# Performance work log

Hardware: AMD Instinct MI355X
Metric: run time of the kernel (lower is better)

## Reference

```python
import jax, jax.numpy as jnp
import numpy as np

N = 8192
IN_F = 256
OUT_F = 64
ALPHA = 0.3  # LeakyReLU negative slope
NEG_INF = -9e15


def setup_inputs() -> dict:
    key = jax.random.key(0)
    k1, k2, k3, k4 = jax.random.split(key, 4)
    h = jax.random.normal(k1, (N, IN_F), dtype=jnp.float32)
    # sparse-ish binary adjacency with self loops (values are 0/1 floats)
    adj = (jax.random.uniform(k2, (N, N)) < 0.05).astype(jnp.float32)
    adj = jnp.maximum(adj, jnp.eye(N, dtype=jnp.float32))
    # xavier_uniform-style scales (gain=1.414)
    w_lim = 1.414 * np.sqrt(6.0 / (IN_F + OUT_F))
    a_lim = 1.414 * np.sqrt(6.0 / (2 * OUT_F + 1))
    W = jax.random.uniform(k3, (IN_F, OUT_F), minval=-w_lim, maxval=w_lim, dtype=jnp.float32)
    a = jax.random.uniform(k4, (2 * OUT_F, 1), minval=-a_lim, maxval=a_lim, dtype=jnp.float32)
    return {"h": h, "adj": adj, "W": W, "a": a}


def reference(h, adj, W, a):
    # Wh: [N, F]
    Wh = h @ W
    # Additive decomposition of the original concat-attention:
    # e_ij = leakyrelu(a[:F].Wh_i + a[F:].Wh_j)  -- identical math, no NxNx2F tensor
    src = Wh @ a[:OUT_F]      # [N, 1]
    dst = Wh @ a[OUT_F:]      # [N, 1]
    e = jax.nn.leaky_relu(src + dst.T, negative_slope=ALPHA)  # [N, N]
    e = e * adj               # faithful: original multiplies by adj before masking
    att = jnp.where(adj > 0, e, NEG_INF)
    att = jax.nn.softmax(att, axis=1)
    # dropout omitted (eval mode / deterministic reference)
    h_prime = att @ Wh        # [N, F]
    return jax.nn.elu(h_prime)
```

## Files before the change

kernel.cpp:

```cpp
#include <hip/hip_runtime.h>
#include <hip/hip_bf16.h>

#define N_NODES 8192
#define IN_F    256
#define OUT_F   64
#define ALPHA   0.3f
#define MBIAS   20.0f
#define CSPL    8
#define COLS_PER (N_NODES / CSPL)
#define NTILES  (COLS_PER / 64)
#define LDP     72

typedef unsigned short u16;
typedef unsigned int   u32;
typedef __attribute__((ext_vector_type(8))) short bf16x8;
typedef __attribute__((ext_vector_type(4))) float f32x4;

__device__ __forceinline__ float bf2f(u32 u) { return __uint_as_float(u << 16); }
__device__ __forceinline__ u32 f2bfbits(float x) {
    u32 u = __float_as_uint(x);
    return (u + 0x7FFFu + ((u >> 16) & 1u)) >> 16;
}
__device__ __forceinline__ float lrelu(float s) { return s > 0.f ? s : ALPHA * s; }

template <bool BF16>
__device__ __forceinline__ float ld(const void* p, size_t idx) {
    if constexpr (BF16) return bf2f(((const u16*)p)[idx]);
    else                return ((const float*)p)[idx];
}

__global__ void gat_detect_kernel(const unsigned* __restrict__ adj_words,
                                  int* __restrict__ flag) {
    *flag = ((adj_words[0] & 0xFFFFu) == 0x3F80u) ? 1 : 0;
}

template <bool BF16>
__device__ __forceinline__ void wh4_impl(
    const void* __restrict__ h, const void* __restrict__ W,
    const void* __restrict__ a, float* __restrict__ src,
    float* __restrict__ dst, int i0, int lane, float* accv)
{
    float acc0 = 0.f, acc1 = 0.f, acc2 = 0.f, acc3 = 0.f;
#pragma unroll 8
    for (int k = 0; k < IN_F; ++k) {
        float wv = ld<BF16>(W, (size_t)k * OUT_F + lane);
        float h0 = ld<BF16>(h, (size_t)(i0 + 0) * IN_F + k);
        float h1 = ld<BF16>(h, (size_t)(i0 + 1) * IN_F + k);
        float h2 = ld<BF16>(h, (size_t)(i0 + 2) * IN_F + k);
        float h3 = ld<BF16>(h, (size_t)(i0 + 3) * IN_F + k);
        acc0 = fmaf(h0, wv, acc0);
        acc1 = fmaf(h1, wv, acc1);
        acc2 = fmaf(h2, wv, acc2);
        acc3 = fmaf(h3, wv, acc3);
    }
    float av = ld<BF16>(a, lane);
    float bv = ld<BF16>(a, OUT_F + lane);
    float accs[4] = {acc0, acc1, acc2, acc3};
#pragma unroll
    for (int r = 0; r < 4; ++r) {
        float ps = accs[r] * av, pd = accs[r] * bv;
#pragma unroll
        for (int off = 32; off > 0; off >>= 1) {
            ps += __shfl_xor(ps, off, 64);
            pd += __shfl_xor(pd, off, 64);
        }
        if (lane == 0) { src[i0 + r] = ps; dst[i0 + r] = pd; }
        accv[r] = accs[r];
    }
}

__global__ __launch_bounds__(256) void gat_wh_kernel(
    const void* __restrict__ h, const void* __restrict__ W,
    const void* __restrict__ a, const int* __restrict__ flag,
    u16* __restrict__ WhT, float* __restrict__ src, float* __restrict__ dst)
{
    __shared__ float accs[16][OUT_F];
    const int tid = threadIdx.x, wave = tid >> 6, lane = tid & 63;
    const int i0 = blockIdx.x * 16 + wave * 4;
    float av[4];
    if (*flag) wh4_impl<true >(h, W, a, src, dst, i0, lane, av);
    else       wh4_impl<false>(h, W, a, src, dst, i0, lane, av);
#pragma unroll
    for (int r = 0; r < 4; ++r) accs[wave * 4 + r][lane] = av[r];
    __syncthreads();
    if (tid < OUT_F) {
        u32 w[8];
#pragma unroll
        for (int e = 0; e < 8; ++e) {
            u32 lo = f2bfbits(accs[2 * e][tid]);
            u32 hi = f2bfbits(accs[2 * e + 1][tid]);
            w[e] = lo | (hi << 16);
        }
        u16* dstp = WhT + (size_t)tid * N_NODES + blockIdx.x * 16;
        *(uint4*)dstp       = *(uint4*)&w[0];
        *(uint4*)(dstp + 8) = *(uint4*)&w[4];
    }
}

template <bool BF16>
__device__ __forceinline__ u32 adj_mask16(const void* adjrow_base, int t)
{
    u32 msk = 0;
    if constexpr (BF16) {
        const uint4* p = (const uint4*)((const u16*)adjrow_base + t * 64);
        uint4 a0 = p[0], a1 = p[1];
        u32 aw[8] = {a0.x, a0.y, a0.z, a0.w, a1.x, a1.y, a1.z, a1.w};
#pragma unroll
        for (int e = 0; e < 8; ++e) {
            if (aw[e] & 0xFFFFu) msk |= (1u << (2 * e));
            if (aw[e] >> 16)     msk |= (1u << (2 * e + 1));
        }
    } else {
        const uint4* p = (const uint4*)((const float*)adjrow_base + t * 64);
        uint4 a0 = p[0], a1 = p[1], a2 = p[2], a3 = p[3];
        u32 aw[16] = {a0.x,a0.y,a0.z,a0.w, a1.x,a1.y,a1.z,a1.w,
                      a2.x,a2.y,a2.z,a2.w, a3.x,a3.y,a3.z,a3.w};
#pragma unroll
        for (int e = 0; e < 16; ++e)
            if (aw[e]) msk |= (1u << e);
    }
    return msk;
}

__global__ __launch_bounds__(256, 4) void gat_attn_kernel(
    const void* __restrict__ adj, const u16* __restrict__ WhT,
    const float* __restrict__ src, const float* __restrict__ dst,
    const int* __restrict__ flag,
    float* __restrict__ O_part, float* __restrict__ l_part)
{
    __shared__ alignas(16) u16 Plds[2][64 * LDP];
    __shared__ alignas(16) u16 Blds[2][64 * LDP];

    const int tid = threadIdx.x, wave = tid >> 6, lane = tid & 63;
    const int r = tid >> 2, cq = tid & 3;
    const int i0 = blockIdx.x * 64, c0 = blockIdx.y * COLS_PER;
    const int isbf = *flag;

    const float srow = src[i0 + r];
    const float m = lrelu(srow + MBIAS);

    const void* adjrow = isbf
        ? (const void*)((const u16*)adj + (size_t)(i0 + r) * N_NODES + c0 + cq * 16)
        : (const void*)((const float*)adj + (size_t)(i0 + r) * N_NODES + c0 + cq * 16);
    const u16*    whtrow = WhT + (size_t)r * N_NODES + c0 + cq * 16;
    const float4* dstp   = (const float4*)(dst + c0 + cq * 16);

    const int mrow = (lane & 15);
    const int kq   = (lane >> 4) * 8;
    const int pw   = r * LDP + cq * 16;

    f32x4 acc[4] = {{0,0,0,0},{0,0,0,0},{0,0,0,0},{0,0,0,0}};
    float lacc = 0.f;

    uint4  pb0, pb1;
    u32    pmsk;
    float4 pd0, pd1, pd2, pd3;

#define LOAD_TILE(t)                                                      \
    do {                                                                  \
        pb0 = *(const uint4*)(whtrow + (t) * 64);                         \
        pb1 = *(const uint4*)(whtrow + (t) * 64 + 8);                     \
        pmsk = isbf ? adj_mask16<true >(adjrow, (t))                      \
                    : adj_mask16<false>(adjrow, (t));                     \
        pd0 = dstp[(t) * 16];     pd1 = dstp[(t) * 16 + 1];               \
        pd2 = dstp[(t) * 16 + 2]; pd3 = dstp[(t) * 16 + 3];               \
    } while (0)

#define STAGE_TILE(buf)                                                   \
    do {                                                                  \
        *(uint4*)&Blds[buf][pw]     = pb0;                                \
        *(uint4*)&Blds[buf][pw + 8] = pb1;                                \
        float dv[16] = {pd0.x,pd0.y,pd0.z,pd0.w, pd1.x,pd1.y,pd1.z,pd1.w, \
                        pd2.x,pd2.y,pd2.z,pd2.w, pd3.x,pd3.y,pd3.z,pd3.w};\
        u32 po[8];                                                        \
        _Pragma("unroll")                                                 \
        for (int e = 0; e < 8; ++e) {                                     \
            float s0 = lrelu(srow + dv[2 * e]);                           \
            float s1 = lrelu(srow + dv[2 * e + 1]);                       \
            float p0 = (pmsk & (1u << (2 * e)))     ? __expf(s0 - m) : 0.f;\
            float p1 = (pmsk & (1u << (2 * e + 1))) ? __expf(s1 - m) : 0.f;\
            u32 q0 = f2bfbits(p0), q1 = f2bfbits(p1);                     \
            lacc += bf2f(q0) + bf2f(q1);            \
            po[e] = q0 | (q1 << 16);                                      \
        }                                                                 \
        *(uint4*)&Plds[buf][pw]     = *(uint4*)&po[0];                    \
        *(uint4*)&Plds[buf][pw + 8] = *(uint4*)&po[4];                    \
    } while (0)

    LOAD_TILE(0);
    STAGE_TILE(0);
    __syncthreads();

    for (int t = 0; t < NTILES; ++t) {
        const int cur = t & 1, nxt = cur ^ 1;
        if (t + 1 < NTILES) LOAD_TILE(t + 1);

#pragma unroll
        for (int ks = 0; ks < 2; ++ks) {
            bf16x8 avf = *(bf16x8*)&Plds[cur][(16 * wave + mrow) * LDP + ks * 32 + kq];
#pragma unroll
            for (int nt = 0; nt < 4; ++nt) {
                bf16x8 bvf = *(bf16x8*)&Blds[cur][(16 * nt + mrow) * LDP + ks * 32 + kq];
                acc[nt] = __builtin_amdgcn_mfma_f32_16x16x32_bf16(avf, bvf, acc[nt], 0, 0, 0);
            }
        }
        if (t + 1 < NTILES) STAGE_TILE(nxt);
        __syncthreads();
    }
#undef LOAD_TILE
#undef STAGE_TILE

    lacc += __shfl_xor(lacc, 1, 64);
    lacc += __shfl_xor(lacc, 2, 64);
    if (cq == 0) l_part[blockIdx.y * N_NODES + i0 + r] = lacc;

    float* Ob = O_part + (size_t)blockIdx.y * N_NODES * OUT_F;
#pragma unroll
    for (int nt = 0; nt < 4; ++nt)
#pragma unroll
        for (int reg = 0; reg < 4; ++reg) {
            int row = i0 + 16 * wave + (lane >> 4) * 4 + reg;
            int col = 16 * nt + (lane & 15);
            Ob[(size_t)row * OUT_F + col] = acc[nt][reg];
        }
}

__global__ __launch_bounds__(256) void gat_reduce_kernel(
    const float* __restrict__ O_part, const float* __restrict__ l_part,
    const int* __restrict__ flag, void* __restrict__ out)
{
    int gid = blockIdx.x * 256 + threadIdx.x;
    int i = gid >> 6;
    float O = 0.f, L = 0.f;
#pragma unroll
    for (int c = 0; c < CSPL; ++c) {
        O += O_part[(size_t)c * N_NODES * OUT_F + gid];
        L += l_part[c * N_NODES + i];
    }
    float hp = O / L;
    float o = hp > 0.f ? hp : expm1f(hp);
    if (*flag) ((u16*)out)[gid] = (u16)f2bfbits(o);
    else       ((float*)out)[gid] = o;
}

extern "C" void kernel_launch(void* const* d_in, const int* in_sizes, int n_in,
                              void* d_out, int out_size, void* d_ws, size_t ws_size,
                              hipStream_t stream)
{
    const void* h   = d_in[0];
    const void* adj = d_in[1];
    const void* W   = d_in[2];
    const void* a   = d_in[3];

    char* ws = (char*)d_ws;
    u16*   WhT    = (u16*)ws;
    float* src    = (float*)(ws + (1u << 20));
    float* dst    = (float*)(ws + (1u << 20) + 32768);
    int*   flag   = (int*)  (ws + (1u << 20) + 65536);
    float* O_part = (float*)(ws + (2u << 20));
    float* l_part = (float*)(ws + (18u << 20));

    gat_detect_kernel<<<1, 1, 0, stream>>>((const unsigned*)adj, flag);
    gat_wh_kernel<<<N_NODES / 16, 256, 0, stream>>>(h, W, a, flag, WhT, src, dst);
    dim3 grid(N_NODES / 64, CSPL);
    gat_attn_kernel<<<grid, 256, 0, stream>>>(adj, WhT, src, dst, flag, O_part, l_part);
    gat_reduce_kernel<<<N_NODES * OUT_F / 256, 256, 0, stream>>>(O_part, l_part, flag, d_out);
}
```

Measured before the change: 442.2 us.

## Shrink attention row tile to 32, drop double buffering, inline dtype detection

The attention kernel now processes 32 rows per block instead of 64. Each of the 8 threads per row handles 8 columns, and the four waves are split as 2 row-tiles by 2 column-pairs. The software-pipelined double-buffered LDS staging is replaced by a single buffer with two barriers per tile, and occupancy hints go from 4 to 8 blocks per CU. The separate detect kernel is removed and each kernel checks the adjacency dtype inline. The aim is more blocks and parallelism for the adj-bandwidth-bound loop and one fewer launch. The cost is that WhT tiles are reloaded by twice as many blocks and load latency is no longer overlapped with compute.

```diff
diff --git a/kernel.cpp b/kernel.cpp
--- a/kernel.cpp
+++ b/kernel.cpp
@@ -9,6 +9,7 @@
 #define CSPL    8
 #define COLS_PER (N_NODES / CSPL)
 #define NTILES  (COLS_PER / 64)
+#define ROWS    32
 #define LDP     72
 
 typedef unsigned short u16;
@@ -23,15 +24,14 @@
 }
 __device__ __forceinline__ float lrelu(float s) { return s > 0.f ? s : ALPHA * s; }
 
+__device__ __forceinline__ int detect_bf16(const void* adj) {
+    return ((((const u32*)adj)[0] & 0xFFFFu) == 0x3F80u) ? 1 : 0;
+}
+
 template <bool BF16>
 __device__ __forceinline__ float ld(const void* p, size_t idx) {
     if constexpr (BF16) return bf2f(((const u16*)p)[idx]);
     else                return ((const float*)p)[idx];
-}
-
-__global__ void gat_detect_kernel(const unsigned* __restrict__ adj_words,
-                                  int* __restrict__ flag) {
-    *flag = ((adj_words[0] & 0xFFFFu) == 0x3F80u) ? 1 : 0;
 }
 
 template <bool BF16>
@@ -71,15 +71,15 @@
 
 __global__ __launch_bounds__(256) void gat_wh_kernel(
     const void* __restrict__ h, const void* __restrict__ W,
-    const void* __restrict__ a, const int* __restrict__ flag,
+    const void* __restrict__ a, const void* __restrict__ adj,
     u16* __restrict__ WhT, float* __restrict__ src, float* __restrict__ dst)
 {
     __shared__ float accs[16][OUT_F];
     const int tid = threadIdx.x, wave = tid >> 6, lane = tid & 63;
     const int i0 = blockIdx.x * 16 + wave * 4;
     float av[4];
-    if (*flag) wh4_impl<true >(h, W, a, src, dst, i0, lane, av);
-    else       wh4_impl<false>(h, W, a, src, dst, i0, lane, av);
+    if (detect_bf16(adj)) wh4_impl<true >(h, W, a, src, dst, i0, lane, av);
+    else                  wh4_impl<false>(h, W, a, src, dst, i0, lane, av);
 #pragma unroll
     for (int r = 0; r < 4; ++r) accs[wave * 4 + r][lane] = av[r];
     __syncthreads();
@@ -97,137 +97,108 @@
     }
 }
 
-template <bool BF16>
-__device__ __forceinline__ u32 adj_mask16(const void* adjrow_base, int t)
-{
-    u32 msk = 0;
-    if constexpr (BF16) {
-        const uint4* p = (const uint4*)((const u16*)adjrow_base + t * 64);
-        uint4 a0 = p[0], a1 = p[1];
-        u32 aw[8] = {a0.x, a0.y, a0.z, a0.w, a1.x, a1.y, a1.z, a1.w};
-#pragma unroll
-        for (int e = 0; e < 8; ++e) {
-            if (aw[e] & 0xFFFFu) msk |= (1u << (2 * e));
-            if (aw[e] >> 16)     msk |= (1u << (2 * e + 1));
-        }
-    } else {
-        const uint4* p = (const uint4*)((const float*)adjrow_base + t * 64);
-        uint4 a0 = p[0], a1 = p[1], a2 = p[2], a3 = p[3];
-        u32 aw[16] = {a0.x,a0.y,a0.z,a0.w, a1.x,a1.y,a1.z,a1.w,
-                      a2.x,a2.y,a2.z,a2.w, a3.x,a3.y,a3.z,a3.w};
-#pragma unroll
-        for (int e = 0; e < 16; ++e)
-            if (aw[e]) msk |= (1u << e);
-    }
-    return msk;
-}
-
-__global__ __launch_bounds__(256, 4) void gat_attn_kernel(
+__global__ __launch_bounds__(256, 8) void gat_attn_kernel(
     const void* __restrict__ adj, const u16* __restrict__ WhT,
     const float* __restrict__ src, const float* __restrict__ dst,
-    const int* __restrict__ flag,
     float* __restrict__ O_part, float* __restrict__ l_part)
 {
-    __shared__ alignas(16) u16 Plds[2][64 * LDP];
-    __shared__ alignas(16) u16 Blds[2][64 * LDP];
+    __shared__ alignas(16) u16 Plds[ROWS * LDP];
+    __shared__ alignas(16) u16 Blds[64 * LDP];
 
     const int tid = threadIdx.x, wave = tid >> 6, lane = tid & 63;
-    const int r = tid >> 2, cq = tid & 3;
-    const int i0 = blockIdx.x * 64, c0 = blockIdx.y * COLS_PER;
-    const int isbf = *flag;
+    const int r  = tid >> 3, cq = tid & 7;
+    const int br = tid >> 2, bq = tid & 3;
+    const int i0 = blockIdx.x * ROWS, c0 = blockIdx.y * COLS_PER;
+    const int isbf = detect_bf16(adj);
 
     const float srow = src[i0 + r];
     const float m = lrelu(srow + MBIAS);
 
-    const void* adjrow = isbf
-        ? (const void*)((const u16*)adj + (size_t)(i0 + r) * N_NODES + c0 + cq * 16)
-        : (const void*)((const float*)adj + (size_t)(i0 + r) * N_NODES + c0 + cq * 16);
-    const u16*    whtrow = WhT + (size_t)r * N_NODES + c0 + cq * 16;
-    const float4* dstp   = (const float4*)(dst + c0 + cq * 16);
-
-    const int mrow = (lane & 15);
-    const int kq   = (lane >> 4) * 8;
-    const int pw   = r * LDP + cq * 16;
-
-    f32x4 acc[4] = {{0,0,0,0},{0,0,0,0},{0,0,0,0},{0,0,0,0}};
+    const u16*    whtrow = WhT + (size_t)br * N_NODES + c0 + bq * 16;
+    const float4* dstp   = (const float4*)(dst + c0 + cq * 8);
+    const u16*    adj16  = (const u16*)adj   + (size_t)(i0 + r) * N_NODES + c0 + cq * 8;
+    const float*  adj32  = (const float*)adj + (size_t)(i0 + r) * N_NODES + c0 + cq * 8;
+
+    const int mw = wave & 1, nw = wave >> 1;
+    const int mrow = lane & 15, kq = (lane >> 4) * 8;
+
+    f32x4 acc[2] = {{0,0,0,0},{0,0,0,0}};
     float lacc = 0.f;
 
-    uint4  pb0, pb1;
-    u32    pmsk;
-    float4 pd0, pd1, pd2, pd3;
-
-#define LOAD_TILE(t)                                                      \
-    do {                                                                  \
-        pb0 = *(const uint4*)(whtrow + (t) * 64);                         \
-        pb1 = *(const uint4*)(whtrow + (t) * 64 + 8);                     \
-        pmsk = isbf ? adj_mask16<true >(adjrow, (t))                      \
-                    : adj_mask16<false>(adjrow, (t));                     \
-        pd0 = dstp[(t) * 16];     pd1 = dstp[(t) * 16 + 1];               \
-        pd2 = dstp[(t) * 16 + 2]; pd3 = dstp[(t) * 16 + 3];               \
-    } while (0)
-
-#define STAGE_TILE(buf)                                                   \
-    do {                                                                  \
-        *(uint4*)&Blds[buf][pw]     = pb0;                                \
-        *(uint4*)&Blds[buf][pw + 8] = pb1;                                \
-        float dv[16] = {pd0.x,pd0.y,pd0.z,pd0.w, pd1.x,pd1.y,pd1.z,pd1.w, \
-                        pd2.x,pd2.y,pd2.z,pd2.w, pd3.x,pd3.y,pd3.z,pd3.w};\
-        u32 po[8];                                                        \
-        _Pragma("unroll")                                                 \
-        for (int e = 0; e < 8; ++e) {                                     \
-            float s0 = lrelu(srow + dv[2 * e]);                           \
-            float s1 = lrelu(srow + dv[2 * e + 1]);                       \
-            float p0 = (pmsk & (1u << (2 * e)))     ? __expf(s0 - m) : 0.f;\
-            float p1 = (pmsk & (1u << (2 * e + 1))) ? __expf(s1 - m) : 0.f;\
-            u32 q0 = f2bfbits(p0), q1 = f2bfbits(p1);                     \
-            lacc += bf2f(q0) + bf2f(q1);            \
-            po[e] = q0 | (q1 << 16);                                      \
-        }                                                                 \
-        *(uint4*)&Plds[buf][pw]     = *(uint4*)&po[0];                    \
-        *(uint4*)&Plds[buf][pw + 8] = *(uint4*)&po[4];                    \
-    } while (0)
-
-    LOAD_TILE(0);
-    STAGE_TILE(0);
-    __syncthreads();
-
     for (int t = 0; t < NTILES; ++t) {
-        const int cur = t & 1, nxt = cur ^ 1;
-        if (t + 1 < NTILES) LOAD_TILE(t + 1);
+        uint4 b0 = *(const uint4*)(whtrow + t * 64);
+        uint4 b1 = *(const uint4*)(whtrow + t * 64 + 8);
+        *(uint4*)&Blds[br * LDP + bq * 16]     = b0;
+        *(uint4*)&Blds[br * LDP + bq * 16 + 8] = b1;
+
+        u32 msk = 0;
+        if (isbf) {
+            uint4 av = *(const uint4*)(adj16 + t * 64);
+            u32 aw[4] = {av.x, av.y, av.z, av.w};
+#pragma unroll
+            for (int e = 0; e < 4; ++e) {
+                if (aw[e] & 0xFFFFu) msk |= (1u << (2 * e));
+                if (aw[e] >> 16)     msk |= (1u << (2 * e + 1));
+            }
+        } else {
+            uint4 a0 = *(const uint4*)(adj32 + t * 64);
+            uint4 a1 = *(const uint4*)(adj32 + t * 64 + 4);
+            u32 aw[8] = {a0.x,a0.y,a0.z,a0.w, a1.x,a1.y,a1.z,a1.w};
+#pragma unroll
+            for (int e = 0; e < 8; ++e)
+                if (aw[e]) msk |= (1u << e);
+        }
+        float4 d0 = dstp[t * 16], d1 = dstp[t * 16 + 1];
+        float dv[8] = {d0.x,d0.y,d0.z,d0.w, d1.x,d1.y,d1.z,d1.w};
+        u32 po[4];
+#pragma unroll
+        for (int e = 0; e < 4; ++e) {
+            float s0 = lrelu(srow + dv[2 * e]);
+            float s1 = lrelu(srow + dv[2 * e + 1]);
+            float p0 = (msk & (1u << (2 * e)))     ? __expf(s0 - m) : 0.f;
+            float p1 = (msk & (1u << (2 * e + 1))) ? __expf(s1 - m) : 0.f;
+            u32 q0 = f2bfbits(p0), q1 = f2bfbits(p1);
+            lacc += bf2f(q0) + bf2f(q1);
+            po[e] = q0 | (q1 << 16);
+        }
+        *(uint4*)&Plds[r * LDP + cq * 8] = *(uint4*)&po[0];
+
+        __syncthreads();
 
 #pragma unroll
         for (int ks = 0; ks < 2; ++ks) {
-            bf16x8 avf = *(bf16x8*)&Plds[cur][(16 * wave + mrow) * LDP + ks * 32 + kq];
-#pragma unroll
-            for (int nt = 0; nt < 4; ++nt) {
-                bf16x8 bvf = *(bf16x8*)&Blds[cur][(16 * nt + mrow) * LDP + ks * 32 + kq];
-                acc[nt] = __builtin_amdgcn_mfma_f32_16x16x32_bf16(avf, bvf, acc[nt], 0, 0, 0);
+            bf16x8 avf = *(bf16x8*)&Plds[(16 * mw + mrow) * LDP + ks * 32 + kq];
+#pragma unroll
+            for (int nt2 = 0; nt2 < 2; ++nt2) {
+                int nt = nw * 2 + nt2;
+                bf16x8 bvf = *(bf16x8*)&Blds[(16 * nt + mrow) * LDP + ks * 32 + kq];
+                acc[nt2] = __builtin_amdgcn_mfma_f32_16x16x32_bf16(avf, bvf, acc[nt2], 0, 0, 0);
             }
         }
-        if (t + 1 < NTILES) STAGE_TILE(nxt);
         __syncthreads();
     }
-#undef LOAD_TILE
-#undef STAGE_TILE
 
     lacc += __shfl_xor(lacc, 1, 64);
     lacc += __shfl_xor(lacc, 2, 64);
+    lacc += __shfl_xor(lacc, 4, 64);
     if (cq == 0) l_part[blockIdx.y * N_NODES + i0 + r] = lacc;
 
     float* Ob = O_part + (size_t)blockIdx.y * N_NODES * OUT_F;
 #pragma unroll
-    for (int nt = 0; nt < 4; ++nt)
+    for (int nt2 = 0; nt2 < 2; ++nt2) {
+        int nt = nw * 2 + nt2;
 #pragma unroll
         for (int reg = 0; reg < 4; ++reg) {
-            int row = i0 + 16 * wave + (lane >> 4) * 4 + reg;
+            int row = i0 + 16 * mw + (lane >> 4) * 4 + reg;
             int col = 16 * nt + (lane & 15);
-            Ob[(size_t)row * OUT_F + col] = acc[nt][reg];
-        }
+            Ob[(size_t)row * OUT_F + col] = acc[nt2][reg];
+        }
+    }
 }
 
 __global__ __launch_bounds__(256) void gat_reduce_kernel(
     const float* __restrict__ O_part, const float* __restrict__ l_part,
-    const int* __restrict__ flag, void* __restrict__ out)
+    const void* __restrict__ adj, void* __restrict__ out)
 {
     int gid = blockIdx.x * 256 + threadIdx.x;
     int i = gid >> 6;
@@ -239,8 +210,8 @@
     }
     float hp = O / L;
     float o = hp > 0.f ? hp : expm1f(hp);
-    if (*flag) ((u16*)out)[gid] = (u16)f2bfbits(o);
-    else       ((float*)out)[gid] = o;
+    if (detect_bf16(adj)) ((u16*)out)[gid] = (u16)f2bfbits(o);
+    else                  ((float*)out)[gid] = o;
 }
 
 extern "C" void kernel_launch(void* const* d_in, const int* in_sizes, int n_in,
@@ -256,13 +227,11 @@
     u16*   WhT    = (u16*)ws;
     float* src    = (float*)(ws + (1u << 20));
     float* dst    = (float*)(ws + (1u << 20) + 32768);
-    int*   flag   = (int*)  (ws + (1u << 20) + 65536);
     float* O_part = (float*)(ws + (2u << 20));
     float* l_part = (float*)(ws + (18u << 20));
 
-    gat_detect_kernel<<<1, 1, 0, stream>>>((const unsigned*)adj, flag);
-    gat_wh_kernel<<<N_NODES / 16, 256, 0, stream>>>(h, W, a, flag, WhT, src, dst);
-    dim3 grid(N_NODES / 64, CSPL);
-    gat_attn_kernel<<<grid, 256, 0, stream>>>(adj, WhT, src, dst, flag, O_part, l_part);
-    gat_reduce_kernel<<<N_NODES * OUT_F / 256, 256, 0, stream>>>(O_part, l_part, flag, d_out);
-}
+    gat_wh_kernel<<<N_NODES / 16, 256, 0, stream>>>(h, W, a, adj, WhT, src, dst);
+    dim3 grid(N_NODES / ROWS, CSPL);
+    gat_attn_kernel<<<grid, 256, 0, stream>>>(adj, WhT, src, dst, O_part, l_part);
+    gat_reduce_kernel<<<N_NODES * OUT_F / 256, 256, 0, stream>>>(O_part, l_part, adj, d_out);
+}
```

After: 441.2 us. About the same (-0.2%).
